# Optimization experiments

Hardware: AMD Instinct MI355X
Metric: run time of the kernel (lower is better)

Reference implementation:

```python
import jax, jax.numpy as jnp
import numpy as np

N = 2              # tree branching factor per axis
DEPTH = 2          # fixed tree depth (uniform octree -> 4^3 leaf grid)
DATA_DIM = 28      # 3 * basis_dim + 1 (SH9 rgb + sigma)
BASIS_DIM = 9
MAX_STEPS = 16     # >= max DDA crossings of the 4^3 leaf grid
STEP_SIZE = 0.001
BG = 1.0           # background_brightness
B = 262144

SH_C0 = 0.28209479177387814
SH_C1 = 0.4886025119029199
SH_C2 = (1.0925484305920792, -1.0925484305920792, 0.31539156525252005,
         -1.0925484305920792, 0.5462742152960396)


def eval_sh9(d):
    # d: [B,3] unit view directions -> [B,9] real SH basis (svox ordering)
    x, y, z = d[..., 0], d[..., 1], d[..., 2]
    return jnp.stack([
        jnp.full_like(x, SH_C0),
        -SH_C1 * y, SH_C1 * z, -SH_C1 * x,
        SH_C2[0] * x * y, SH_C2[1] * y * z,
        SH_C2[2] * (2.0 * z * z - x * x - y * y),
        SH_C2[3] * x * z, SH_C2[4] * (x * x - y * y),
    ], axis=-1)


def dda_unit(cen, invdir):
    # ray/unit-cube intersection; cen,invdir: [B,3] -> (tmin[B]>=0, tmax[B])
    t1 = -cen * invdir
    t2 = t1 + invdir
    tmin = jnp.maximum(jnp.max(jnp.minimum(t1, t2), axis=-1), 0.0)
    tmax = jnp.minimum(jnp.min(jnp.maximum(t1, t2), axis=-1), 1e9)
    return tmin, tmax


def tree_query(pos, data, child):
    # pos: [B,3] in [0,1); returns leaf values [B,DATA_DIM], corner [B,3], length [B]
    nb = pos.shape[0]
    node = jnp.zeros((nb,), jnp.int32)
    cur = pos
    corner = jnp.zeros_like(pos)
    length = jnp.ones((nb,), pos.dtype)
    done = jnp.zeros((nb,), bool)
    val = jnp.zeros((nb, DATA_DIM), pos.dtype)
    for _ in range(DEPTH):
        idx = jnp.clip(jnp.floor(cur * N).astype(jnp.int32), 0, N - 1)
        ch = child[node, idx[:, 0], idx[:, 1], idx[:, 2]]
        v = data[node, idx[:, 0], idx[:, 1], idx[:, 2]]
        new_len = length / N
        new_corner = corner + idx.astype(pos.dtype) * new_len[:, None]
        upd = ~done
        val = jnp.where(upd[:, None], v, val)
        corner = jnp.where(upd[:, None], new_corner, corner)
        length = jnp.where(upd, new_len, length)
        cur = jnp.where(upd[:, None], cur * N - idx.astype(pos.dtype), cur)
        node = jnp.where(upd, node + ch, node)
        done = done | (ch == 0)
    return val, corner, length


def setup_inputs() -> dict:
    key = jax.random.key(0)
    k0, k1, k2 = jax.random.split(key, 3)
    origins = (jax.random.uniform(k0, (B, 3), jnp.float32) - 0.5) * 0.6
    dirs = jax.random.normal(k1, (B, 3), jnp.float32)
    viewdirs = dirs / jnp.linalg.norm(dirs, axis=-1, keepdims=True)
    n_nodes = 1 + N ** 3
    data = jax.random.normal(k2, (n_nodes, N, N, N, DATA_DIM), jnp.float32) * 0.5
    child = np.zeros((n_nodes, N, N, N), np.int32)
    child[0] = np.arange(1, 1 + N ** 3, dtype=np.int32).reshape(N, N, N)  # relative offsets
    return {
        'origins': origins, 'dirs': dirs, 'viewdirs': viewdirs,
        'data': data, 'child': jnp.asarray(child),
        'offset': jnp.full((3,), 0.5, jnp.float32),
        'invradius': jnp.float32(0.5),
    }


def reference(origins, dirs, viewdirs, data, child, offset, invradius):
    origins_t = offset + origins * invradius          # world2tree
    dirs_n = dirs / jnp.linalg.norm(dirs, axis=-1, keepdims=True)
    invdirs = 1.0 / (dirs_n + 1e-9)
    t, tmax = dda_unit(origins_t, invdirs)
    sh_mult = eval_sh9(viewdirs)                      # [B,9]
    delta_scale = 1.0 / invradius
    light = jnp.ones((origins.shape[0],), origins.dtype)
    out = jnp.zeros((origins.shape[0], 3), origins.dtype)

    def step(carry, _):
        t, light, out = carry
        active = t < tmax
        pos = origins_t + t[:, None] * dirs_n
        pos_c = jnp.clip(pos, 0.0, 1.0 - 1e-6)
        val, corner, length = tree_query(pos_c, data, child)
        pos_local = (pos - corner) / length[:, None]
        smin, smax = dda_unit(pos_local, invdirs)
        delta_t = (smax - smin) * length + STEP_SIZE
        sigma = jax.nn.relu(val[:, -1])
        att = jnp.exp(-delta_t * sigma * delta_scale)
        weight = light * (1.0 - att)
        rgb_sh = val[:, :-1].reshape(-1, 3, BASIS_DIM)
        rgb = jax.nn.sigmoid(jnp.sum(sh_mult[:, None, :] * rgb_sh, axis=-1))
        w = jnp.where(active, weight, 0.0)
        out = out + w[:, None] * rgb
        light = jnp.where(active, light * att, light)
        t = jnp.where(active, t + delta_t, t)
        return (t, light, out), None

    (t, light, out), _ = jax.lax.scan(step, (t, light, out), None, length=MAX_STEPS)
    return out + light[:, None] * BG
```

## Files before the change

### kernel.cpp

```cpp
#include <hip/hip_runtime.h>
#include <math.h>

typedef _Float16 f16;
typedef _Float16 f16x2 __attribute__((ext_vector_type(2)));

constexpr int   DATA_DIM  = 28;
constexpr int   MAX_STEPS = 16;
constexpr float STEP_SIZE = 0.001f;
constexpr float BG        = 1.0f;
constexpr int   CELLS     = 8;
constexpr int   NVOX      = 64;
constexpr int   VOX_H     = 28;

__device__ __forceinline__ float fdot2(unsigned w, f16x2 s, float acc) {
#if __has_builtin(__builtin_amdgcn_fdot2)
    return __builtin_amdgcn_fdot2(__builtin_bit_cast(f16x2, w), s, acc, false);
#else
    f16x2 a = __builtin_bit_cast(f16x2, w);
    return acc + (float)a.x * (float)s.x + (float)a.y * (float)s.y;
#endif
}

#define GEOM(TC, LIDX, DTV)                                                  \
  {                                                                          \
    float px = fmaf((TC), dnx, otx);                                         \
    float py = fmaf((TC), dny, oty);                                         \
    float pz = fmaf((TC), dnz, otz);                                         \
    float pcx = fminf(fmaxf(px, 0.0f), 0.999999f);                           \
    float pcy = fminf(fmaxf(py, 0.0f), 0.999999f);                           \
    float pcz = fminf(fmaxf(pz, 0.0f), 0.999999f);                           \
    int vx = (int)(pcx * 4.0f);                                              \
    int vy = (int)(pcy * 4.0f);                                              \
    int vz = (int)(pcz * 4.0f);                                              \
    (LIDX) = (vx << 4) | (vy << 2) | vz;                                     \
    bool d2 = (d2mask >> (LIDX)) & 1ull;                                     \
    float invlen = d2 ? 4.0f : 2.0f;                                         \
    float lenv   = d2 ? 0.25f : 0.5f;                                        \
    int   shf    = d2 ? 0 : 1;                                               \
    float cfx = (float)(vx >> shf);                                          \
    float cfy = (float)(vy >> shf);                                          \
    float cfz = (float)(vz >> shf);                                          \
    float plx = fmaf(px, invlen, -cfx);                                      \
    float ply = fmaf(py, invlen, -cfy);                                      \
    float plz = fmaf(pz, invlen, -cfz);                                      \
    float t1x = -plx * ivx, t2x = t1x + ivx;                                 \
    float t1y = -ply * ivy, t2y = t1y + ivy;                                 \
    float t1z = -plz * ivz, t2z = t1z + ivz;                                 \
    float mn = fmaxf(fmaxf(fminf(t1x,t2x), fminf(t1y,t2y)), fminf(t1z,t2z)); \
    float mx = fminf(fminf(fmaxf(t1x,t2x), fmaxf(t1y,t2y)), fmaxf(t1z,t2z)); \
    float smin = fmaxf(mn, 0.0f);                                            \
    float smax = fminf(mx, 1000000000.0f);                                   \
    (DTV) = fmaf(smax - smin, lenv, STEP_SIZE);                              \
  }

#define PREF(LI, Q0,Q1,Q2,Q3,Q4,Q5,Q6)                                       \
  {                                                                          \
    const uint2* _r = (const uint2*)(s_vh + (LI) * VOX_H);                   \
    Q0=_r[0]; Q1=_r[1]; Q2=_r[2]; Q3=_r[3]; Q4=_r[4]; Q5=_r[5]; Q6=_r[6];   \
  }

#define STEP(QA0,QA1,QA2,QA3,QA4,QA5,QA6, QB0,QB1,QB2,QB3,QB4,QB5,QB6)      \
  {                                                                          \
    bool act = t_cur < tmax;                                                 \
    if (!__any(act)) break;                                                  \
    float t_next = act ? t_cur + dtc : t_cur;                                \
    int lin; float dtn;                                                      \
    GEOM(t_next, lin, dtn);                                                  \
    PREF(lin, QB0,QB1,QB2,QB3,QB4,QB5,QB6);                                  \
    unsigned D0=QA0.x, D1=QA0.y, D2=QA1.x, D3=QA1.y, D4=QA2.x, D5=QA2.y,     \
             D6=QA3.x, D7=QA3.y, D8=QA4.x, D9=QA4.y, D10=QA5.x, D11=QA5.y,   \
             D12=QA6.x, D13=QA6.y;                                           \
    float a0=0.f, a1=0.f, a2=0.f;                                            \
    a0=fdot2(D0,shA0,a0); a0=fdot2(D1,shA1,a0); a0=fdot2(D2,shA2,a0);        \
    a0=fdot2(D3,shA3,a0); a0=fdot2(D4,shA4,a0);                              \
    a1=fdot2(D4,shB0,a1); a1=fdot2(D5,shB1,a1); a1=fdot2(D6,shB2,a1);        \
    a1=fdot2(D7,shB3,a1); a1=fdot2(D8,shB4,a1);                              \
    a2=fdot2(D9,shA0,a2); a2=fdot2(D10,shA1,a2); a2=fdot2(D11,shA2,a2);      \
    a2=fdot2(D12,shA3,a2); a2=fdot2(D13,shA4,a2);                            \
    f16x2 lastp = __builtin_bit_cast(f16x2, D13);                            \
    float sigma = fmaxf((float)lastp.y, 0.0f);                               \
    float att = __expf(katt * dtc * sigma);                                  \
    float weight = light * (1.0f - att);                                     \
    float w = act ? weight : 0.0f;                                           \
    float r0 = __builtin_amdgcn_rcpf(1.0f + __expf(-a0));                    \
    float r1 = __builtin_amdgcn_rcpf(1.0f + __expf(-a1));                    \
    float r2 = __builtin_amdgcn_rcpf(1.0f + __expf(-a2));                    \
    o0 = fmaf(w, r0, o0);                                                    \
    o1 = fmaf(w, r1, o1);                                                    \
    o2 = fmaf(w, r2, o2);                                                    \
    light = act ? light * att : light;                                       \
    t_cur = t_next;                                                          \
    dtc = dtn;                                                               \
  }

__global__ __launch_bounds__(256) void vr_kernel(
    const float* __restrict__ origins,
    const float* __restrict__ dirs,
    const float* __restrict__ viewdirs,
    const float* __restrict__ data,
    const int*   __restrict__ child,
    const float* __restrict__ offset,
    const float* __restrict__ invradius_p,
    float* __restrict__ out,
    int B)
{
    __shared__ f16 s_vh[NVOX * VOX_H];
    __shared__ int s_fent[NVOX];

    const int t0   = threadIdx.x;
    const int lane = t0 & 63;

    unsigned long long d2mask;
    {
        int vx = lane >> 4, vy = (lane >> 2) & 3, vz = lane & 3;
        int e0 = ((vx >> 1) << 2) | ((vy >> 1) << 1) | (vz >> 1);
        int ch = child[e0];
        d2mask = __ballot(ch != 0);
    }

    if (t0 < NVOX) {
        int vx = t0 >> 4, vy = (t0 >> 2) & 3, vz = t0 & 3;
        int e0 = ((vx >> 1) << 2) | ((vy >> 1) << 1) | (vz >> 1);
        int ch = child[e0];
        int fe = (ch != 0) ? ch * CELLS + (((vx & 1) << 2) | ((vy & 1) << 1) | (vz & 1))
                           : e0;
        s_fent[t0] = fe;
    }
    __syncthreads();
    for (int i = t0; i < NVOX * VOX_H; i += 256) {
        int v = i / VOX_H, j = i - v * VOX_H;
        s_vh[i] = (f16)data[s_fent[v] * DATA_DIM + j];
    }
    __syncthreads();

    int tid = blockIdx.x * 256 + t0;
    if (tid >= B) return;

    float ox = origins[tid*3+0], oy = origins[tid*3+1], oz = origins[tid*3+2];
    float dx = dirs[tid*3+0],    dy = dirs[tid*3+1],    dz = dirs[tid*3+2];
    float vdx = viewdirs[tid*3+0], vdy = viewdirs[tid*3+1], vdz = viewdirs[tid*3+2];
    float invr = invradius_p[0];
    float otx = offset[0] + ox * invr;
    float oty = offset[1] + oy * invr;
    float otz = offset[2] + oz * invr;

    float sh[9];
    {
        const float C0 = 0.28209479177387814f;
        const float C1 = 0.4886025119029199f;
        sh[0] = C0;
        sh[1] = -C1 * vdy;
        sh[2] =  C1 * vdz;
        sh[3] = -C1 * vdx;
        sh[4] =  1.0925484305920792f * vdx * vdy;
        sh[5] = -1.0925484305920792f * vdy * vdz;
        sh[6] =  0.31539156525252005f * (2.0f*vdz*vdz - vdx*vdx - vdy*vdy);
        sh[7] = -1.0925484305920792f * vdx * vdz;
        sh[8] =  0.5462742152960396f * (vdx*vdx - vdy*vdy);
    }
    f16x2 shA0 = f16x2{(f16)sh[0], (f16)sh[1]};
    f16x2 shA1 = f16x2{(f16)sh[2], (f16)sh[3]};
    f16x2 shA2 = f16x2{(f16)sh[4], (f16)sh[5]};
    f16x2 shA3 = f16x2{(f16)sh[6], (f16)sh[7]};
    f16x2 shA4 = f16x2{(f16)sh[8], (f16)0.0f};
    f16x2 shB0 = f16x2{(f16)0.0f,  (f16)sh[0]};
    f16x2 shB1 = f16x2{(f16)sh[1], (f16)sh[2]};
    f16x2 shB2 = f16x2{(f16)sh[3], (f16)sh[4]};
    f16x2 shB3 = f16x2{(f16)sh[5], (f16)sh[6]};
    f16x2 shB4 = f16x2{(f16)sh[7], (f16)sh[8]};

    float nrm = sqrtf(dx*dx + dy*dy + dz*dz);
    float dnx = dx / nrm, dny = dy / nrm, dnz = dz / nrm;
    float ivx = 1.0f / (dnx + 1e-9f);
    float ivy = 1.0f / (dny + 1e-9f);
    float ivz = 1.0f / (dnz + 1e-9f);

    float t_cur, tmax;
    {
        float t1x = -otx * ivx, t2x = t1x + ivx;
        float t1y = -oty * ivy, t2y = t1y + ivy;
        float t1z = -otz * ivz, t2z = t1z + ivz;
        float mn = fmaxf(fmaxf(fminf(t1x,t2x), fminf(t1y,t2y)), fminf(t1z,t2z));
        float mx = fminf(fminf(fmaxf(t1x,t2x), fmaxf(t1y,t2y)), fmaxf(t1z,t2z));
        t_cur = fmaxf(mn, 0.0f);
        tmax  = fminf(mx, 1000000000.0f);
    }

    const float katt = -(1.0f / invr);
    float light = 1.0f;
    float o0 = 0.0f, o1 = 0.0f, o2 = 0.0f;

    uint2 A0,A1,A2,A3,A4,A5,A6, B0,B1,B2,B3,B4,B5,B6;
    int li0; float dtc;
    GEOM(t_cur, li0, dtc);
    PREF(li0, A0,A1,A2,A3,A4,A5,A6);

    #pragma unroll
    for (int s = 0; s < MAX_STEPS; s += 2) {
        STEP(A0,A1,A2,A3,A4,A5,A6, B0,B1,B2,B3,B4,B5,B6);
        STEP(B0,B1,B2,B3,B4,B5,B6, A0,A1,A2,A3,A4,A5,A6);
    }

    out[tid*3+0] = fmaf(light, BG, o0);
    out[tid*3+1] = fmaf(light, BG, o1);
    out[tid*3+2] = fmaf(light, BG, o2);
}

extern "C" void kernel_launch(void* const* d_in, const int* in_sizes, int n_in,
                              void* d_out, int out_size, void* d_ws, size_t ws_size,
                              hipStream_t stream) {
    const float* origins  = (const float*)d_in[0];
    const float* dirs     = (const float*)d_in[1];
    const float* viewdirs = (const float*)d_in[2];
    const float* data     = (const float*)d_in[3];
    const int*   child    = (const int*)d_in[4];
    const float* offset   = (const float*)d_in[5];
    const float* invrad   = (const float*)d_in[6];
    float* out = (float*)d_out;
    int B = in_sizes[0] / 3;
    int block = 256;
    int grid = (B + block - 1) / block;
    vr_kernel<<<grid, block, 0, stream>>>(origins, dirs, viewdirs, data, child,
                                          offset, invrad, out, B);
}
```

Baseline: 13.98 us.

## Fold log2e into SH and attenuation, simplify DDA, vectorize LDS fill, 512-thread blocks

Pre-scales the SH coefficients and attenuation constant by -log2(e) so the sigmoid and attenuation use a raw exp2. The per-step DDA is rewritten in world-space units with precomputed scaled inverse directions, removing the local-coordinate transform and the final length multiply. The shared-memory voxel table is filled in one pass with float4 loads and half4 stores, dropping a barrier and the integer division. Blocks grow to 512 threads with launch bounds (512,4), the early-exit check moves to once per pair of steps, and the step loop is no longer unrolled, which trades code size for loop overhead. Folding the scale into half-precision SH values and skipping one wave-wide check per pair changes rounding and can run one extra masked step.

```diff
diff --git a/kernel.cpp b/kernel.cpp
--- a/kernel.cpp
+++ b/kernel.cpp
@@ -3,14 +3,15 @@
 
 typedef _Float16 f16;
 typedef _Float16 f16x2 __attribute__((ext_vector_type(2)));
-
-constexpr int   DATA_DIM  = 28;
+typedef _Float16 f16x4 __attribute__((ext_vector_type(4)));
+
 constexpr int   MAX_STEPS = 16;
 constexpr float STEP_SIZE = 0.001f;
 constexpr float BG        = 1.0f;
-constexpr int   CELLS     = 8;
 constexpr int   NVOX      = 64;
 constexpr int   VOX_H     = 28;
+constexpr float NLOG2E    = -1.4426950408889634f;
+constexpr float BIGT      = 2.4e8f;
 
 __device__ __forceinline__ float fdot2(unsigned w, f16x2 s, float acc) {
 #if __has_builtin(__builtin_amdgcn_fdot2)
@@ -18,6 +19,14 @@
 #else
     f16x2 a = __builtin_bit_cast(f16x2, w);
     return acc + (float)a.x * (float)s.x + (float)a.y * (float)s.y;
+#endif
+}
+
+__device__ __forceinline__ float fexp2(float x) {
+#if __has_builtin(__builtin_amdgcn_exp2f)
+    return __builtin_amdgcn_exp2f(x);
+#else
+    return exp2f(x);
 #endif
 }
 
@@ -34,35 +43,30 @@
     int vz = (int)(pcz * 4.0f);                                              \
     (LIDX) = (vx << 4) | (vy << 2) | vz;                                     \
     bool d2 = (d2mask >> (LIDX)) & 1ull;                                     \
-    float invlen = d2 ? 4.0f : 2.0f;                                         \
-    float lenv   = d2 ? 0.25f : 0.5f;                                        \
-    int   shf    = d2 ? 0 : 1;                                               \
-    float cfx = (float)(vx >> shf);                                          \
-    float cfy = (float)(vy >> shf);                                          \
-    float cfz = (float)(vz >> shf);                                          \
-    float plx = fmaf(px, invlen, -cfx);                                      \
-    float ply = fmaf(py, invlen, -cfy);                                      \
-    float plz = fmaf(pz, invlen, -cfz);                                      \
-    float t1x = -plx * ivx, t2x = t1x + ivx;                                 \
-    float t1y = -ply * ivy, t2y = t1y + ivy;                                 \
-    float t1z = -plz * ivz, t2z = t1z + ivz;                                 \
-    float mn = fmaxf(fmaxf(fminf(t1x,t2x), fminf(t1y,t2y)), fminf(t1z,t2z)); \
-    float mx = fminf(fminf(fmaxf(t1x,t2x), fmaxf(t1y,t2y)), fmaxf(t1z,t2z)); \
-    float smin = fmaxf(mn, 0.0f);                                            \
-    float smax = fminf(mx, 1000000000.0f);                                   \
-    (DTV) = fmaf(smax - smin, lenv, STEP_SIZE);                              \
+    float lenv = d2 ? 0.25f : 0.5f;                                          \
+    int   shf  = d2 ? 0 : 1;                                                 \
+    float T1x = fmaf((float)(vx >> shf), lenv, -px) * ivx;                   \
+    float T1y = fmaf((float)(vy >> shf), lenv, -py) * ivy;                   \
+    float T1z = fmaf((float)(vz >> shf), lenv, -pz) * ivz;                   \
+    float T2x = T1x + (d2 ? ivqx : ivhx);                                    \
+    float T2y = T1y + (d2 ? ivqy : ivhy);                                    \
+    float T2z = T1z + (d2 ? ivqz : ivhz);                                    \
+    float m = fmaxf(fmaxf(fminf(T1x,T2x), fminf(T1y,T2y)),                   \
+                    fmaxf(fminf(T1z,T2z), 0.0f));                            \
+    float M = fminf(fminf(fmaxf(T1x,T2x), fmaxf(T1y,T2y)),                   \
+                    fminf(fmaxf(T1z,T2z), BIGT));                            \
+    (DTV) = (M - m) + STEP_SIZE;                                             \
   }
 
 #define PREF(LI, Q0,Q1,Q2,Q3,Q4,Q5,Q6)                                       \
   {                                                                          \
     const uint2* _r = (const uint2*)(s_vh + (LI) * VOX_H);                   \
-    Q0=_r[0]; Q1=_r[1]; Q2=_r[2]; Q3=_r[3]; Q4=_r[4]; Q5=_r[5]; Q6=_r[6];   \
+    Q0=_r[0]; Q1=_r[1]; Q2=_r[2]; Q3=_r[3]; Q4=_r[4]; Q5=_r[5]; Q6=_r[6];    \
   }
 
-#define STEP(QA0,QA1,QA2,QA3,QA4,QA5,QA6, QB0,QB1,QB2,QB3,QB4,QB5,QB6)      \
+#define STEP(QA0,QA1,QA2,QA3,QA4,QA5,QA6, QB0,QB1,QB2,QB3,QB4,QB5,QB6)       \
   {                                                                          \
     bool act = t_cur < tmax;                                                 \
-    if (!__any(act)) break;                                                  \
     float t_next = act ? t_cur + dtc : t_cur;                                \
     int lin; float dtn;                                                      \
     GEOM(t_next, lin, dtn);                                                  \
@@ -70,7 +74,7 @@
     unsigned D0=QA0.x, D1=QA0.y, D2=QA1.x, D3=QA1.y, D4=QA2.x, D5=QA2.y,     \
              D6=QA3.x, D7=QA3.y, D8=QA4.x, D9=QA4.y, D10=QA5.x, D11=QA5.y,   \
              D12=QA6.x, D13=QA6.y;                                           \
-    float a0=0.f, a1=0.f, a2=0.f;                                            \
+    float a0=0.f, a1=0.f, a2=0.f;             \
     a0=fdot2(D0,shA0,a0); a0=fdot2(D1,shA1,a0); a0=fdot2(D2,shA2,a0);        \
     a0=fdot2(D3,shA3,a0); a0=fdot2(D4,shA4,a0);                              \
     a1=fdot2(D4,shB0,a1); a1=fdot2(D5,shB1,a1); a1=fdot2(D6,shB2,a1);        \
@@ -79,21 +83,21 @@
     a2=fdot2(D12,shA3,a2); a2=fdot2(D13,shA4,a2);                            \
     f16x2 lastp = __builtin_bit_cast(f16x2, D13);                            \
     float sigma = fmaxf((float)lastp.y, 0.0f);                               \
-    float att = __expf(katt * dtc * sigma);                                  \
-    float weight = light * (1.0f - att);                                     \
-    float w = act ? weight : 0.0f;                                           \
-    float r0 = __builtin_amdgcn_rcpf(1.0f + __expf(-a0));                    \
-    float r1 = __builtin_amdgcn_rcpf(1.0f + __expf(-a1));                    \
-    float r2 = __builtin_amdgcn_rcpf(1.0f + __expf(-a2));                    \
+    float att = fexp2(katt2 * dtc * sigma);                                  \
+    float la  = light * att;                                                 \
+    float w   = act ? (light - la) : 0.0f;                                   \
+    float r0 = __builtin_amdgcn_rcpf(1.0f + fexp2(a0));                      \
+    float r1 = __builtin_amdgcn_rcpf(1.0f + fexp2(a1));                      \
+    float r2 = __builtin_amdgcn_rcpf(1.0f + fexp2(a2));                      \
     o0 = fmaf(w, r0, o0);                                                    \
     o1 = fmaf(w, r1, o1);                                                    \
     o2 = fmaf(w, r2, o2);                                                    \
-    light = act ? light * att : light;                                       \
+    light = act ? la : light;                                                \
     t_cur = t_next;                                                          \
     dtc = dtn;                                                               \
   }
 
-__global__ __launch_bounds__(256) void vr_kernel(
+__global__ __launch_bounds__(512, 4) void vr_kernel(
     const float* __restrict__ origins,
     const float* __restrict__ dirs,
     const float* __restrict__ viewdirs,
@@ -105,7 +109,6 @@
     int B)
 {
     __shared__ f16 s_vh[NVOX * VOX_H];
-    __shared__ int s_fent[NVOX];
 
     const int t0   = threadIdx.x;
     const int lane = t0 & 63;
@@ -114,26 +117,25 @@
     {
         int vx = lane >> 4, vy = (lane >> 2) & 3, vz = lane & 3;
         int e0 = ((vx >> 1) << 2) | ((vy >> 1) << 1) | (vz >> 1);
-        int ch = child[e0];
-        d2mask = __ballot(ch != 0);
-    }
-
-    if (t0 < NVOX) {
-        int vx = t0 >> 4, vy = (t0 >> 2) & 3, vz = t0 & 3;
-        int e0 = ((vx >> 1) << 2) | ((vy >> 1) << 1) | (vz >> 1);
-        int ch = child[e0];
-        int fe = (ch != 0) ? ch * CELLS + (((vx & 1) << 2) | ((vy & 1) << 1) | (vz & 1))
-                           : e0;
-        s_fent[t0] = fe;
+        d2mask = __ballot(child[e0] != 0);
+    }
+
+    {
+        int v = t0 >> 3, s = t0 & 7;
+        if (v < NVOX && s < 7) {
+            int vx = v >> 4, vy = (v >> 2) & 3, vz = v & 3;
+            int e0  = ((vx >> 1) << 2) | ((vy >> 1) << 1) | (vz >> 1);
+            int ch  = child[e0];
+            int fe  = ch ? ch * 8 + (((vx & 1) << 2) | ((vy & 1) << 1) | (vz & 1))
+                         : e0;
+            float4 w = *reinterpret_cast<const float4*>(data + fe * 28 + s * 4);
+            f16x4 p; p.x=(f16)w.x; p.y=(f16)w.y; p.z=(f16)w.z; p.w=(f16)w.w;
+            *reinterpret_cast<f16x4*>(s_vh + v * VOX_H + s * 4) = p;
+        }
     }
     __syncthreads();
-    for (int i = t0; i < NVOX * VOX_H; i += 256) {
-        int v = i / VOX_H, j = i - v * VOX_H;
-        s_vh[i] = (f16)data[s_fent[v] * DATA_DIM + j];
-    }
-    __syncthreads();
-
-    int tid = blockIdx.x * 256 + t0;
+
+    int tid = blockIdx.x * 512 + t0;
     if (tid >= B) return;
 
     float ox = origins[tid*3+0], oy = origins[tid*3+1], oz = origins[tid*3+2];
@@ -157,6 +159,8 @@
         sh[6] =  0.31539156525252005f * (2.0f*vdz*vdz - vdx*vdx - vdy*vdy);
         sh[7] = -1.0925484305920792f * vdx * vdz;
         sh[8] =  0.5462742152960396f * (vdx*vdx - vdy*vdy);
+        #pragma unroll
+        for (int k = 0; k < 9; ++k) sh[k] *= NLOG2E;
     }
     f16x2 shA0 = f16x2{(f16)sh[0], (f16)sh[1]};
     f16x2 shA1 = f16x2{(f16)sh[2], (f16)sh[3]};
@@ -174,6 +178,8 @@
     float ivx = 1.0f / (dnx + 1e-9f);
     float ivy = 1.0f / (dny + 1e-9f);
     float ivz = 1.0f / (dnz + 1e-9f);
+    float ivqx = ivx * 0.25f, ivqy = ivy * 0.25f, ivqz = ivz * 0.25f;
+    float ivhx = ivx * 0.5f,  ivhy = ivy * 0.5f,  ivhz = ivz * 0.5f;
 
     float t_cur, tmax;
     {
@@ -186,7 +192,7 @@
         tmax  = fminf(mx, 1000000000.0f);
     }
 
-    const float katt = -(1.0f / invr);
+    const float katt2 = (1.0f / invr) * NLOG2E;
     float light = 1.0f;
     float o0 = 0.0f, o1 = 0.0f, o2 = 0.0f;
 
@@ -195,8 +201,9 @@
     GEOM(t_cur, li0, dtc);
     PREF(li0, A0,A1,A2,A3,A4,A5,A6);
 
-    #pragma unroll
+    #pragma unroll 1
     for (int s = 0; s < MAX_STEPS; s += 2) {
+        if (!__any(t_cur < tmax)) break;
         STEP(A0,A1,A2,A3,A4,A5,A6, B0,B1,B2,B3,B4,B5,B6);
         STEP(B0,B1,B2,B3,B4,B5,B6, A0,A1,A2,A3,A4,A5,A6);
     }
@@ -218,7 +225,7 @@
     const float* invrad   = (const float*)d_in[6];
     float* out = (float*)d_out;
     int B = in_sizes[0] / 3;
-    int block = 256;
+    int block = 512;
     int grid = (B + block - 1) / block;
     vr_kernel<<<grid, block, 0, stream>>>(origins, dirs, viewdirs, data, child,
                                           offset, invrad, out, B);
```

Result: no change. 14.08 us (+0.7%).
